# Performance work log

Hardware: AMD Instinct MI355X
Metric: run time of the kernel (lower is better)

Reference implementation:

```python
import jax, jax.numpy as jnp
import numpy as np

N = 50000
E = 1600000
IN_C = 128
HID = 64
OUT_C = 64
EPS = 1e-5
NEG_SLOPE = 0.01  # nn.LeakyReLU default


def setup_inputs() -> dict:
    key = jax.random.key(0)
    ks = jax.random.split(key, 8)
    x = jax.random.normal(ks[0], (N, IN_C), dtype=jnp.float32)
    x_e = jnp.zeros((1,), dtype=jnp.float32)  # unused by the module
    edge_index = jax.random.randint(ks[1], (2, E), 0, N, dtype=jnp.int64)
    # Parameters (torch default-ish init scale)
    s1 = 1.0 / np.sqrt(IN_C)
    W1 = jax.random.uniform(ks[2], (HID, IN_C), jnp.float32, -s1, s1)
    b1 = jax.random.uniform(ks[3], (HID,), jnp.float32, -s1, s1)
    gamma = jnp.ones((HID,), jnp.float32)
    beta = jnp.zeros((HID,), jnp.float32)
    s2 = 1.0 / np.sqrt(HID)
    W2 = jax.random.uniform(ks[4], (OUT_C, HID), jnp.float32, -s2, s2)
    b2 = jax.random.uniform(ks[5], (OUT_C,), jnp.float32, -s2, s2)
    return {"x": x, "x_e": x_e, "edge_index": edge_index,
            "W1": W1, "b1": b1, "gamma": gamma, "beta": beta,
            "W2": W2, "b2": b2}


def reference(x, x_e, edge_index, W1, b1, gamma, beta, W2, b2):
    # dropout: identity in eval mode
    h = jax.nn.leaky_relu(x @ W1.T + b1, negative_slope=NEG_SLOPE)  # [N, HID]
    # LayerNorm over last dim
    mu = jnp.mean(h, axis=-1, keepdims=True)
    var = jnp.mean(jnp.square(h - mu), axis=-1, keepdims=True)
    h = (h - mu) * jax.lax.rsqrt(var + EPS) * gamma + beta
    # gather over src edges, scatter-min into dst nodes
    src, dst = edge_index[0], edge_index[1]
    agg = jax.ops.segment_min(h[src], dst, num_segments=N)  # [N, HID]
    # nodes with no incoming edge: segment_min -> +inf; PyG fills 0
    agg = jnp.where(jnp.isinf(agg), 0.0, agg)
    out = agg @ W2.T + b2  # [N, OUT_C]
    return out
```

## Files before the change

### kernel.cpp

```cpp
#include <hip/hip_runtime.h>
#include <hip/hip_fp16.h>
#include <cstdint>
#include <math.h>

#define IN_C 128
#define HID 64
#define OUT_C 64
#define EPS_LN 1e-5f
#define NEG_SLOPE 0.01f

#define NBUCKET 1024
#define ROWS 49
#define CAP 2048
#define EPB 4096

typedef __attribute__((ext_vector_type(8))) short short8;
typedef __attribute__((ext_vector_type(4))) float f32x4;
typedef __attribute__((ext_vector_type(2))) _Float16 f16x2;

__device__ __forceinline__ float bcastf(float v, int l) {
    return __int_as_float(__builtin_amdgcn_readlane(__float_as_int(v), l));
}
__device__ __forceinline__ unsigned bcastu(unsigned v, int l) {
    return (unsigned)__builtin_amdgcn_readlane((int)v, l);
}
__device__ __forceinline__ unsigned pack_hi(float f0, float f1) {
    return (__float_as_uint(f0) >> 16) | (__float_as_uint(f1) & 0xFFFF0000u);
}
__device__ __forceinline__ float hi_part(float f) {
    return __uint_as_float(__float_as_uint(f) & 0xFFFF0000u);
}
__device__ __forceinline__ unsigned hmin2u(unsigned a, unsigned b) {
#if __has_builtin(__builtin_elementwise_min)
    union { unsigned u; f16x2 v; } ua, ub, r;
    ua.u = a; ub.u = b;
    r.v = __builtin_elementwise_min(ua.v, ub.v);
    return r.u;
#else
    union { unsigned u; __half2_raw h2; } ua, ub, r;
    ua.u = a; ub.u = b;
    __half lo = __hmin(__half(__half_raw{ua.h2.x}), __half(__half_raw{ub.h2.x}));
    __half hi = __hmin(__half(__half_raw{ua.h2.y}), __half(__half_raw{ub.h2.y}));
    r.h2.x = __half_raw(lo).data; r.h2.y = __half_raw(hi).data;
    return r.u;
#endif
}

__global__ __launch_bounds__(256) void mlp_ln_mfma_kernel(
    const float* __restrict__ x, const float* __restrict__ W1,
    const float* __restrict__ b1, const float* __restrict__ gamma,
    const float* __restrict__ beta, unsigned short* __restrict__ h16,
    unsigned* __restrict__ cursor, int N)
{
    __shared__ unsigned whi[64 * 68];
    __shared__ unsigned wlo[64 * 68];
    __shared__ unsigned short hT[64 * 66];

    const int tid = threadIdx.x;

    if (blockIdx.x == 0) {
        for (int i = tid; i < NBUCKET; i += 256) cursor[i * 16] = 0;
    }

    {
        int r = tid >> 2, q = tid & 3;
        const float4* wr4 = (const float4*)(W1 + r * IN_C + q * 32);
#pragma unroll
        for (int p = 0; p < 8; ++p) {
            float4 f = wr4[p];
            unsigned h0 = pack_hi(f.x, f.y);
            unsigned h1 = pack_hi(f.z, f.w);
            unsigned l0 = pack_hi(f.x - hi_part(f.x), f.y - hi_part(f.y));
            unsigned l1 = pack_hi(f.z - hi_part(f.z), f.w - hi_part(f.w));
            whi[r * 68 + q * 16 + 2 * p]     = h0;
            whi[r * 68 + q * 16 + 2 * p + 1] = h1;
            wlo[r * 68 + q * 16 + 2 * p]     = l0;
            wlo[r * 68 + q * 16 + 2 * p + 1] = l1;
        }
    }
    __syncthreads();

    const int lane = tid & 63;
    const int w    = tid >> 6;
    const int col  = lane & 15;
    const int g    = lane >> 4;
    const int nodeBase0 = blockIdx.x * 64;
    const int nodeBase  = nodeBase0 + w * 16;

    f32x4 acc[4];
#pragma unroll
    for (int t = 0; t < 4; ++t) acc[t] = (f32x4){0.f, 0.f, 0.f, 0.f};

    const int nodeCl = min(nodeBase + col, N - 1);

#pragma unroll
    for (int ks = 0; ks < 4; ++ks) {
        const float* xp = x + (size_t)nodeCl * IN_C + ks * 32 + g * 8;
        float4 fa = *(const float4*)xp;
        float4 fb = *(const float4*)(xp + 4);
        float f[8] = {fa.x, fa.y, fa.z, fa.w, fb.x, fb.y, fb.z, fb.w};
        union { unsigned u[4]; short8 s; } Ah, Al;
#pragma unroll
        for (int p = 0; p < 4; ++p) {
            float f0 = f[2 * p], f1 = f[2 * p + 1];
            Ah.u[p] = pack_hi(f0, f1);
            Al.u[p] = pack_hi(f0 - hi_part(f0), f1 - hi_part(f1));
        }
#pragma unroll
        for (int t = 0; t < 4; ++t) {
            const short8* bh = (const short8*)&whi[(t * 16 + col) * 68 + ks * 16 + g * 4];
            const short8* bl = (const short8*)&wlo[(t * 16 + col) * 68 + ks * 16 + g * 4];
            short8 Bh = *bh;
            short8 Bl = *bl;
            acc[t] = __builtin_amdgcn_mfma_f32_16x16x32_bf16(Ah.s, Bh, acc[t], 0, 0, 0);
            acc[t] = __builtin_amdgcn_mfma_f32_16x16x32_bf16(Ah.s, Bl, acc[t], 0, 0, 0);
            acc[t] = __builtin_amdgcn_mfma_f32_16x16x32_bf16(Al.s, Bh, acc[t], 0, 0, 0);
        }
    }

    float b1v[4], gv[4], bv[4];
#pragma unroll
    for (int t = 0; t < 4; ++t) {
        b1v[t] = b1[t * 16 + col];
        gv[t]  = gamma[t * 16 + col];
        bv[t]  = beta[t * 16 + col];
    }
    float val[4][4];
#pragma unroll
    for (int t = 0; t < 4; ++t)
#pragma unroll
        for (int r = 0; r < 4; ++r) {
            float v = acc[t][r] + b1v[t];
            val[t][r] = v > 0.f ? v : v * NEG_SLOPE;
        }

    float s[4], q[4];
#pragma unroll
    for (int r = 0; r < 4; ++r) {
        s[r] = val[0][r] + val[1][r] + val[2][r] + val[3][r];
        q[r] = fmaf(val[0][r], val[0][r],
               fmaf(val[1][r], val[1][r],
               fmaf(val[2][r], val[2][r], val[3][r] * val[3][r])));
    }
#pragma unroll
    for (int off = 1; off < 16; off <<= 1) {
#pragma unroll
        for (int r = 0; r < 4; ++r) {
            s[r] += __shfl_xor(s[r], off, 64);
            q[r] += __shfl_xor(q[r], off, 64);
        }
    }
    float mu[4], rstd[4];
#pragma unroll
    for (int r = 0; r < 4; ++r) {
        mu[r] = s[r] * (1.f / 64.f);
        float var = q[r] * (1.f / 64.f) - mu[r] * mu[r];
        rstd[r] = rsqrtf(var + EPS_LN);
    }
#pragma unroll
    for (int t = 0; t < 4; ++t)
#pragma unroll
        for (int r = 0; r < 4; ++r) {
            float hn = (val[t][r] - mu[r]) * rstd[r] * gv[t] + bv[t];
            int nodeL = w * 16 + g * 4 + r;
            hT[nodeL * 66 + t * 16 + col] = __half_as_ushort(__float2half(hn));
        }
    __syncthreads();

    {
        int nodeL = tid >> 2, part = tid & 3;
        int node = nodeBase0 + nodeL;
        if (node < N) {
            const unsigned* hrow = (const unsigned*)hT;
            unsigned tmp[8];
#pragma unroll
            for (int i = 0; i < 8; ++i) tmp[i] = hrow[nodeL * 33 + part * 8 + i];
            unsigned* gp = (unsigned*)h16 + (size_t)node * 32 + part * 8;
            *(uint4*)gp       = (uint4){tmp[0], tmp[1], tmp[2], tmp[3]};
            *(uint4*)(gp + 4) = (uint4){tmp[4], tmp[5], tmp[6], tmp[7]};
        }
    }
}

__global__ __launch_bounds__(512) void bucket_scatter_kernel(
    const int* __restrict__ ei, unsigned* __restrict__ cursor ,
    unsigned* __restrict__ pairs, int E)
{
    __shared__ unsigned hist[NBUCKET];
    __shared__ unsigned run_start[NBUCKET];
    __shared__ unsigned c2[NBUCKET];
    __shared__ unsigned gbase[NBUCKET];
    __shared__ unsigned pre[512];
    __shared__ unsigned staged[EPB];
    __shared__ unsigned short bof[EPB];

    const int tid = threadIdx.x;
    const int base = blockIdx.x * EPB;

    hist[tid] = 0;
    hist[tid + 512] = 0;
    __syncthreads();

    unsigned pk[8];
    unsigned short bk[8];
#pragma unroll
    for (int k = 0; k < 8; ++k) {
        int e = base + k * 512 + tid;
        if (e < E) {
            unsigned src = (unsigned)ei[e];
            unsigned dst = (unsigned)ei[E + e];
            unsigned b = dst & (NBUCKET - 1);
            pk[k] = src | ((dst >> 10) << 16);
            bk[k] = (unsigned short)b;
            atomicAdd(&hist[b], 1u);
        } else {
            bk[k] = 0xFFFFu;
        }
    }
    __syncthreads();

    unsigned sA = hist[2 * tid], sB = hist[2 * tid + 1];
    pre[tid] = sA + sB;
    __syncthreads();
    for (int off = 1; off < 512; off <<= 1) {
        unsigned v = (tid >= off) ? pre[tid - off] : 0u;
        __syncthreads();
        pre[tid] += v;
        __syncthreads();
    }
    unsigned excl = pre[tid] - (sA + sB);
    run_start[2 * tid] = excl;
    run_start[2 * tid + 1] = excl + sA;
    c2[2 * tid] = excl;
    c2[2 * tid + 1] = excl + sA;
    if (sA) gbase[2 * tid] = atomicAdd(&cursor[(2 * tid) * 16], sA);
    if (sB) gbase[2 * tid + 1] = atomicAdd(&cursor[(2 * tid + 1) * 16], sB);
    __syncthreads();

#pragma unroll
    for (int k = 0; k < 8; ++k) {
        if (bk[k] != 0xFFFFu) {
            unsigned pos = atomicAdd(&c2[bk[k]], 1u);
            staged[pos] = pk[k];
            bof[pos] = bk[k];
        }
    }
    __syncthreads();

    int total = min(EPB, E - base);
    for (int i = tid; i < total; i += 512) {
        unsigned b = bof[i];
        unsigned local = gbase[b] + ((unsigned)i - run_start[b]);
        if (local < CAP) pairs[(size_t)b * CAP + local] = staged[i];
    }
}

__global__ __launch_bounds__(512) void bucket_reduce_gemm_kernel(
    const unsigned* __restrict__ hp ,
    const unsigned* __restrict__ cursor, const unsigned* __restrict__ pairs,
    const float* __restrict__ W2, const float* __restrict__ b2,
    float* __restrict__ out, int N)
{
    __shared__ unsigned rec_sorted[CAP];
    __shared__ unsigned accP[ROWS * 33];
    __shared__ float w2t[HID * 65];
    __shared__ unsigned rhist[64], rstart[64], rc[64];

    const int tid  = threadIdx.x;
    const int lane = tid & 63;
    const int wid  = tid >> 6;
    const int hsel = lane >> 5;
    const unsigned c = (unsigned)(lane & 31);
    const unsigned b = blockIdx.x;

    if (tid < 64) rhist[tid] = 0;
    for (int m = tid; m < OUT_C * HID; m += 512) {
        int o = m >> 6, j = m & 63;
        w2t[j * 65 + o] = W2[m];
    }

    const unsigned cnt = min(cursor[b * 16], (unsigned)CAP);
    unsigned myrec[4];
#pragma unroll
    for (int k = 0; k < 4; ++k) {
        unsigned i = (unsigned)tid + k * 512;
        myrec[k] = (i < cnt) ? pairs[(size_t)b * CAP + i] : 0xFFFFFFFFu;
    }
    __syncthreads();

#pragma unroll
    for (int k = 0; k < 4; ++k)
        if (myrec[k] != 0xFFFFFFFFu) atomicAdd(&rhist[myrec[k] >> 16], 1u);
    __syncthreads();

    if (wid == 0) {
        unsigned v = (lane < ROWS) ? rhist[lane] : 0u;
        unsigned inc = v;
#pragma unroll
        for (int off = 1; off < 64; off <<= 1) {
            unsigned u = __shfl_up(inc, (unsigned)off, 64);
            if (lane >= off) inc += u;
        }
        if (lane < ROWS) { rstart[lane] = inc - v; rc[lane] = inc - v; }
    }
    __syncthreads();

#pragma unroll
    for (int k = 0; k < 4; ++k)
        if (myrec[k] != 0xFFFFFFFFu) {
            unsigned pos = atomicAdd(&rc[myrec[k] >> 16], 1u);
            rec_sorted[pos] = myrec[k];
        }
    __syncthreads();

    const unsigned INITV = 0x7C007C00u;
    for (int r = wid; r < ROWS; r += 8) {
        unsigned st = rstart[r];
        unsigned L  = rhist[r];
        unsigned m0 = INITV, m1 = INITV;
        for (unsigned bb = 0; bb < L; bb += 64) {
            int mm = (int)min(64u, L - bb);
            unsigned recs = (lane < mm) ? rec_sorted[st + bb + lane] : 0u;
            int j = 0;
            for (; j + 4 <= mm; j += 4) {
                unsigned rA = bcastu(recs, j + 0), rB = bcastu(recs, j + 1);
                unsigned rC = bcastu(recs, j + 2), rD = bcastu(recs, j + 3);
                unsigned n0 = (hsel ? rB : rA) & 0xFFFFu;
                unsigned n1 = (hsel ? rD : rC) & 0xFFFFu;
                unsigned v0 = hp[(size_t)n0 * 32 + c];
                unsigned v1 = hp[(size_t)n1 * 32 + c];
                m0 = hmin2u(m0, v0);
                m1 = hmin2u(m1, v1);
            }
            for (; j + 2 <= mm; j += 2) {
                unsigned rA = bcastu(recs, j), rB = bcastu(recs, j + 1);
                unsigned n0 = (hsel ? rB : rA) & 0xFFFFu;
                m0 = hmin2u(m0, hp[(size_t)n0 * 32 + c]);
            }
            if (j < mm) {
                unsigned rA = bcastu(recs, j);
                unsigned n0 = rA & 0xFFFFu;
                m0 = hmin2u(m0, hp[(size_t)n0 * 32 + c]);
            }
        }
        unsigned rm = hmin2u(m0, m1);
        unsigned ot = __shfl_xor(rm, 32, 64);
        rm = hmin2u(rm, ot);
        if (hsel == 0) accP[r * 33 + c] = rm;
    }
    __syncthreads();

    const float b2l = b2[lane];
    for (int r = wid; r < ROWS; r += 8) {
        int dst = (r << 10) | (int)b;
        if (dst >= N) continue;
        unsigned pv = accP[r * 33 + (lane >> 1)];
        unsigned short key = (lane & 1) ? (unsigned short)(pv >> 16)
                                        : (unsigned short)(pv & 0xFFFFu);
        float a = (key == 0x7C00) ? 0.f : __half2float(__ushort_as_half(key));
        float o = b2l;
#pragma unroll
        for (int j = 0; j < 64; ++j)
            o = fmaf(bcastf(a, j), w2t[j * 65 + lane], o);
        out[(size_t)dst * OUT_C + lane] = o;
    }
}

extern "C" void kernel_launch(void* const* d_in, const int* in_sizes, int n_in,
                              void* d_out, int out_size, void* d_ws, size_t ws_size,
                              hipStream_t stream) {
    const float* x     = (const float*)d_in[0];
    const int*   ei    = (const int*)d_in[2];
    const float* W1    = (const float*)d_in[3];
    const float* b1    = (const float*)d_in[4];
    const float* gamma = (const float*)d_in[5];
    const float* beta  = (const float*)d_in[6];
    const float* W2    = (const float*)d_in[7];
    const float* b2    = (const float*)d_in[8];
    float* out = (float*)d_out;

    const int N = in_sizes[0] / IN_C;
    const int E = in_sizes[2] / 2;

    unsigned short* h16 = (unsigned short*)d_ws;
    unsigned* pairs  = (unsigned*)(h16 + (size_t)N * HID);
    unsigned* cursor = pairs + (size_t)NBUCKET * CAP;

    const int mlp_blocks = (N + 63) / 64;
    mlp_ln_mfma_kernel<<<mlp_blocks, 256, 0, stream>>>(
        x, W1, b1, gamma, beta, h16, cursor, N);

    const int scat_blocks = (E + EPB - 1) / EPB;
    bucket_scatter_kernel<<<scat_blocks, 512, 0, stream>>>(ei, cursor, pairs, E);

    bucket_reduce_gemm_kernel<<<NBUCKET, 512, 0, stream>>>(
        (const unsigned*)h16, cursor, pairs, W2, b2, out, N);
}
```

Before: 170.2 us.

## Vectorize bucket gather-min with 16-byte loads and use MFMA for output GEMM

The gather-min loop now has each wave process 8 edges at a time, with each lane loading 16 bytes (4 packed half2) of the source row. Partial minima are combined with xor-shuffles, replacing the per-edge readlane broadcast and 4-byte loads. The final 49x64 by 64x64 projection now runs on fp16 MFMA (16x16x32) from LDS tiles instead of a scalar fma loop with readlane broadcasts. W2 is converted to fp16, which lowers the precision of the output projection. Inf entries are zeroed before the GEMM.

```diff
diff --git a/kernel.cpp b/kernel.cpp
--- a/kernel.cpp
+++ b/kernel.cpp
@@ -17,13 +17,8 @@
 typedef __attribute__((ext_vector_type(8))) short short8;
 typedef __attribute__((ext_vector_type(4))) float f32x4;
 typedef __attribute__((ext_vector_type(2))) _Float16 f16x2;
-
-__device__ __forceinline__ float bcastf(float v, int l) {
-    return __int_as_float(__builtin_amdgcn_readlane(__float_as_int(v), l));
-}
-__device__ __forceinline__ unsigned bcastu(unsigned v, int l) {
-    return (unsigned)__builtin_amdgcn_readlane((int)v, l);
-}
+typedef __attribute__((ext_vector_type(8))) _Float16 f16x8;
+
 __device__ __forceinline__ unsigned pack_hi(float f0, float f1) {
     return (__float_as_uint(f0) >> 16) | (__float_as_uint(f1) & 0xFFFF0000u);
 }
@@ -31,19 +26,10 @@
     return __uint_as_float(__float_as_uint(f) & 0xFFFF0000u);
 }
 __device__ __forceinline__ unsigned hmin2u(unsigned a, unsigned b) {
-#if __has_builtin(__builtin_elementwise_min)
     union { unsigned u; f16x2 v; } ua, ub, r;
     ua.u = a; ub.u = b;
     r.v = __builtin_elementwise_min(ua.v, ub.v);
     return r.u;
-#else
-    union { unsigned u; __half2_raw h2; } ua, ub, r;
-    ua.u = a; ub.u = b;
-    __half lo = __hmin(__half(__half_raw{ua.h2.x}), __half(__half_raw{ub.h2.x}));
-    __half hi = __hmin(__half(__half_raw{ua.h2.y}), __half(__half_raw{ub.h2.y}));
-    r.h2.x = __half_raw(lo).data; r.h2.y = __half_raw(hi).data;
-    return r.u;
-#endif
 }
 
 __global__ __launch_bounds__(256) void mlp_ln_mfma_kernel(
@@ -262,21 +248,25 @@
     float* __restrict__ out, int N)
 {
     __shared__ unsigned rec_sorted[CAP];
-    __shared__ unsigned accP[ROWS * 33];
-    __shared__ float w2t[HID * 65];
+    __shared__ unsigned accP[64 * 36];
+    __shared__ unsigned w2h[64 * 36];
     __shared__ unsigned rhist[64], rstart[64], rc[64];
 
     const int tid  = threadIdx.x;
     const int lane = tid & 63;
     const int wid  = tid >> 6;
-    const int hsel = lane >> 5;
-    const unsigned c = (unsigned)(lane & 31);
     const unsigned b = blockIdx.x;
+    const unsigned INITV = 0x7C007C00u;
 
     if (tid < 64) rhist[tid] = 0;
-    for (int m = tid; m < OUT_C * HID; m += 512) {
-        int o = m >> 6, j = m & 63;
-        w2t[j * 65 + o] = W2[m];
+    for (int i = tid; i < 64 * 36; i += 512) accP[i] = INITV;
+    for (int i = tid; i < 64 * 32; i += 512) {
+        int n = i >> 5, p = i & 5 * 6 + 1;
+        p = i & 31;
+        float f0 = W2[n * 64 + 2 * p], f1 = W2[n * 64 + 2 * p + 1];
+        unsigned u0 = (unsigned)__half_as_ushort(__float2half(f0));
+        unsigned u1 = (unsigned)__half_as_ushort(__float2half(f1));
+        w2h[n * 36 + p] = u0 | (u1 << 16);
     }
 
     const unsigned cnt = min(cursor[b * 16], (unsigned)CAP);
@@ -313,56 +303,70 @@
         }
     __syncthreads();
 
-    const unsigned INITV = 0x7C007C00u;
+    const unsigned sub = (unsigned)(lane >> 3);
+    const unsigned cg  = (unsigned)(lane & 7);
     for (int r = wid; r < ROWS; r += 8) {
+        unsigned L = rhist[r];
+        if (L == 0) continue;
         unsigned st = rstart[r];
-        unsigned L  = rhist[r];
-        unsigned m0 = INITV, m1 = INITV;
-        for (unsigned bb = 0; bb < L; bb += 64) {
-            int mm = (int)min(64u, L - bb);
-            unsigned recs = (lane < mm) ? rec_sorted[st + bb + lane] : 0u;
-            int j = 0;
-            for (; j + 4 <= mm; j += 4) {
-                unsigned rA = bcastu(recs, j + 0), rB = bcastu(recs, j + 1);
-                unsigned rC = bcastu(recs, j + 2), rD = bcastu(recs, j + 3);
-                unsigned n0 = (hsel ? rB : rA) & 0xFFFFu;
-                unsigned n1 = (hsel ? rD : rC) & 0xFFFFu;
-                unsigned v0 = hp[(size_t)n0 * 32 + c];
-                unsigned v1 = hp[(size_t)n1 * 32 + c];
-                m0 = hmin2u(m0, v0);
-                m1 = hmin2u(m1, v1);
+        uint4 acc = {INITV, INITV, INITV, INITV};
+        for (unsigned bb = 0; bb < L; bb += 8) {
+            unsigned k = bb + sub;
+            unsigned rec = rec_sorted[st + min(k, L - 1)];
+            unsigned node = rec & 0xFFFFu;
+            uint4 v = *(const uint4*)(hp + (size_t)node * 32 + cg * 4);
+            acc.x = hmin2u(acc.x, v.x);
+            acc.y = hmin2u(acc.y, v.y);
+            acc.z = hmin2u(acc.z, v.z);
+            acc.w = hmin2u(acc.w, v.w);
+        }
+#pragma unroll
+        for (int off = 8; off < 64; off <<= 1) {
+            acc.x = hmin2u(acc.x, (unsigned)__shfl_xor((int)acc.x, off, 64));
+            acc.y = hmin2u(acc.y, (unsigned)__shfl_xor((int)acc.y, off, 64));
+            acc.z = hmin2u(acc.z, (unsigned)__shfl_xor((int)acc.z, off, 64));
+            acc.w = hmin2u(acc.w, (unsigned)__shfl_xor((int)acc.w, off, 64));
+        }
+        if (lane < 8)
+            *(uint4*)&accP[r * 36 + cg * 4] = acc;
+    }
+    __syncthreads();
+
+    for (int i = tid; i < 64 * 32; i += 512) {
+        int r = i >> 5, p = i & 31;
+        unsigned v = accP[r * 36 + p];
+        unsigned lo = v & 0xFFFFu, hi = v >> 16;
+        if (lo == 0x7C00u) lo = 0;
+        if (hi == 0x7C00u) hi = 0;
+        accP[r * 36 + p] = lo | (hi << 16);
+    }
+    __syncthreads();
+
+    {
+        const int col = lane & 15;
+        const int g   = lane >> 4;
+        const int mtile = wid >> 1;
+        f16x8 afrag[2];
+#pragma unroll
+        for (int kt = 0; kt < 2; ++kt)
+            afrag[kt] = *(const f16x8*)&accP[(mtile * 16 + col) * 36 + kt * 16 + g * 4];
+#pragma unroll
+        for (int nn = 0; nn < 2; ++nn) {
+            int ntile = (wid & 1) * 2 + nn;
+            f16x8 b0 = *(const f16x8*)&w2h[(ntile * 16 + col) * 36 + 0 * 16 + g * 4];
+            f16x8 b1f = *(const f16x8*)&w2h[(ntile * 16 + col) * 36 + 1 * 16 + g * 4];
+            f32x4 c = {0.f, 0.f, 0.f, 0.f};
+            c = __builtin_amdgcn_mfma_f32_16x16x32_f16(afrag[0], b0, c, 0, 0, 0);
+            c = __builtin_amdgcn_mfma_f32_16x16x32_f16(afrag[1], b1f, c, 0, 0, 0);
+            float b2v = b2[ntile * 16 + col];
+#pragma unroll
+            for (int r4 = 0; r4 < 4; ++r4) {
+                int m = mtile * 16 + g * 4 + r4;
+                int dst = (m << 10) | (int)b;
+                if (m < ROWS && dst < N)
+                    out[(size_t)dst * OUT_C + ntile * 16 + col] = c[r4] + b2v;
             }
-            for (; j + 2 <= mm; j += 2) {
-                unsigned rA = bcastu(recs, j), rB = bcastu(recs, j + 1);
-                unsigned n0 = (hsel ? rB : rA) & 0xFFFFu;
-                m0 = hmin2u(m0, hp[(size_t)n0 * 32 + c]);
-            }
-            if (j < mm) {
-                unsigned rA = bcastu(recs, j);
-                unsigned n0 = rA & 0xFFFFu;
-                m0 = hmin2u(m0, hp[(size_t)n0 * 32 + c]);
-            }
-        }
-        unsigned rm = hmin2u(m0, m1);
-        unsigned ot = __shfl_xor(rm, 32, 64);
-        rm = hmin2u(rm, ot);
-        if (hsel == 0) accP[r * 33 + c] = rm;
-    }
-    __syncthreads();
-
-    const float b2l = b2[lane];
-    for (int r = wid; r < ROWS; r += 8) {
-        int dst = (r << 10) | (int)b;
-        if (dst >= N) continue;
-        unsigned pv = accP[r * 33 + (lane >> 1)];
-        unsigned short key = (lane & 1) ? (unsigned short)(pv >> 16)
-                                        : (unsigned short)(pv & 0xFFFFu);
-        float a = (key == 0x7C00) ? 0.f : __half2float(__ushort_as_half(key));
-        float o = b2l;
-#pragma unroll
-        for (int j = 0; j < 64; ++j)
-            o = fmaf(bcastf(a, j), w2t[j * 65 + lane], o);
-        out[(size_t)dst * OUT_C + lane] = o;
+        }
     }
 }
 
```

Result: faster. 147.2 us (-13.5%).
